# Optimization experiments

Measured on AMD Instinct MI355X. Metric: run time of the kernel, lower is better.

The kernel has to match this reference:

```python
import jax, jax.numpy as jnp
import numpy as np

B, N, D_IN, D_OUT = 16, 512, 256, 32
C_SP, H, W = 64, 256, 256


def setup_inputs() -> dict:
    key = jax.random.key(0)
    k1, k2, k3, k4, k5 = jax.random.split(key, 5)
    return {
        "spatial_info": jax.random.normal(k1, (B, C_SP, H, W), dtype=jnp.float32),
        "entity_embeddings": jax.random.normal(k2, (B, N, D_IN), dtype=jnp.float32),
        "W_proj": jax.random.normal(k3, (D_IN, D_OUT), dtype=jnp.float32) / np.sqrt(D_IN),
        "b_proj": jax.random.normal(k4, (D_OUT,), dtype=jnp.float32) * 0.01,
        "locations": jax.random.randint(k5, (B, N, 2), 0, 256, dtype=jnp.int32),
    }


def reference(spatial_info, entity_embeddings, W_proj, b_proj, locations):
    # per-entity linear projection (fc_block): [B, N, D_out]
    proj = jnp.einsum('bnd,de->bne', entity_embeddings, W_proj) + b_proj

    Bb, C, Hh, Ww = spatial_info.shape
    # clamp locations like the torch min/max logic
    h = jnp.clip(locations[..., 0], 0, Hh - 1)  # [B, N]
    w = jnp.clip(locations[..., 1], 0, Ww - 1)  # [B, N]
    flat = h * Ww + w                            # [B, N] flattened spatial index

    scatter_map = jnp.zeros((Bb, Hh * Ww, proj.shape[-1]), dtype=spatial_info.dtype)
    b_idx = jnp.arange(Bb, dtype=flat.dtype)[:, None]  # [B, 1]
    scatter_map = scatter_map.at[b_idx, flat].set(proj)
    scatter_map = scatter_map.reshape(Bb, Hh, Ww, -1).transpose(0, 3, 1, 2)  # [B, D_out, H, W]

    return jnp.concatenate([spatial_info, scatter_map], axis=1)
```

## Files before the change

### kernel.cpp

```cpp
#include <hip/hip_runtime.h>

#define BATCH 16
#define NENT  512
#define D_IN  256
#define D_OUT 32
#define CSP   64
#define COUT  96
#define HWDIM 256
#define HWSZ  65536
#define HW4   16384
#define SP_B4  (CSP * HW4)
#define SC_B4  (D_OUT * HW4)
#define OUT_B4 (COUT * HW4)

__global__ void init_proj_kernel(const float* __restrict__ emb,
                                 const float* __restrict__ Wp,
                                 const float* __restrict__ bp,
                                 int4* __restrict__ owner4,
                                 float* __restrict__ projbuf) {
    int tid = blockIdx.x * blockDim.x + threadIdx.x;
    const int NZ4 = BATCH * HWSZ / 4;
    if (tid < NZ4) {
        owner4[tid] = make_int4(0, 0, 0, 0);
        return;
    }
    int gid = tid - NZ4;
    int ent = gid >> 5;
    int e   = gid & 31;
    float acc = bp[e];
    const float* er = emb + ent * D_IN;
    #pragma unroll 8
    for (int d = 0; d < D_IN; ++d) {
        acc += er[d] * Wp[d * D_OUT + e];
    }
    projbuf[gid] = acc;
}

__global__ void owner_kernel(const int* __restrict__ loc,
                             int* __restrict__ owner) {
    int gid = blockIdx.x * blockDim.x + threadIdx.x;
    if (gid >= BATCH * NENT) return;
    int h = loc[gid * 2 + 0];
    int w = loc[gid * 2 + 1];
    h = min(max(h, 0), HWDIM - 1);
    w = min(max(w, 0), HWDIM - 1);
    int b = gid >> 9;
    int n = gid & (NENT - 1);
    atomicMax(&owner[b * HWSZ + h * HWDIM + w], n + 1);
}

__global__ void fused_out_kernel(const float4* __restrict__ sp,
                                 const int4* __restrict__ owner4,
                                 const float* __restrict__ projbuf,
                                 float4* __restrict__ out) {
    const int PER = 2048 * 256;
    int b = blockIdx.y;
    int t = blockIdx.x * blockDim.x + threadIdx.x;

    const float4* spb  = sp  + (size_t)b * SP_B4;
    float4*       outb = out + (size_t)b * OUT_B4;

    outb[t]        = spb[t];
    outb[t + PER]  = spb[t + PER];

    int e   = t >> 14;
    int hw4 = t & (HW4 - 1);
    int4 ow = owner4[b * HW4 + hw4];
    const float* pb = projbuf + b * (NENT * D_OUT) + e;
    float4 v;
    v.x = ow.x ? pb[(ow.x - 1) * D_OUT] : 0.f;
    v.y = ow.y ? pb[(ow.y - 1) * D_OUT] : 0.f;
    v.z = ow.z ? pb[(ow.z - 1) * D_OUT] : 0.f;
    v.w = ow.w ? pb[(ow.w - 1) * D_OUT] : 0.f;
    outb[SP_B4 + t] = v;
}

extern "C" void kernel_launch(void* const* d_in, const int* in_sizes, int n_in,
                              void* d_out, int out_size, void* d_ws, size_t ws_size,
                              hipStream_t stream) {
    const float* spatial = (const float*)d_in[0];
    const float* emb     = (const float*)d_in[1];
    const float* Wp      = (const float*)d_in[2];
    const float* bp      = (const float*)d_in[3];
    const int*   loc     = (const int*)d_in[4];
    float* out = (float*)d_out;

    int*   owner   = (int*)d_ws;
    float* projbuf = (float*)((char*)d_ws + BATCH * HWSZ * sizeof(int));

    init_proj_kernel<<<2048, 256, 0, stream>>>(emb, Wp, bp, (int4*)owner, projbuf);
    owner_kernel<<<32, 256, 0, stream>>>(loc, owner);
    dim3 grid(2048, BATCH);
    fused_out_kernel<<<grid, 256, 0, stream>>>((const float4*)spatial,
                                               (const int4*)owner, projbuf,
                                               (float4*)out);
}
```

Before: 143.4 us.

## Use nontemporal loads/stores for streaming copy and vectorize projection embedding loads

The spatial copy and scatter output stores now use nontemporal load/store builtins so the large streamed data bypasses cache retention. The projection GEMV reads embedding rows as float4 vectors, and the gather loads are made unconditional with a clamped index so they can be issued without branching. The aim is less cache pollution in the bandwidth-bound copy and fewer load instructions, at the cost of extra speculative gather loads for empty cells.

```diff
diff --git a/kernel.cpp b/kernel.cpp
--- a/kernel.cpp
+++ b/kernel.cpp
@@ -13,25 +13,34 @@
 #define SC_B4  (D_OUT * HW4)
 #define OUT_B4 (COUT * HW4)
 
+typedef float vfloat4 __attribute__((ext_vector_type(4)));
+typedef int   vint4   __attribute__((ext_vector_type(4)));
+
 __global__ void init_proj_kernel(const float* __restrict__ emb,
                                  const float* __restrict__ Wp,
                                  const float* __restrict__ bp,
-                                 int4* __restrict__ owner4,
+                                 vint4* __restrict__ owner4,
                                  float* __restrict__ projbuf) {
     int tid = blockIdx.x * blockDim.x + threadIdx.x;
     const int NZ4 = BATCH * HWSZ / 4;
     if (tid < NZ4) {
-        owner4[tid] = make_int4(0, 0, 0, 0);
+        vint4 z = {0, 0, 0, 0};
+        owner4[tid] = z;
         return;
     }
     int gid = tid - NZ4;
     int ent = gid >> 5;
     int e   = gid & 31;
+    const vfloat4* er4 = (const vfloat4*)(emb + (size_t)ent * D_IN);
     float acc = bp[e];
-    const float* er = emb + ent * D_IN;
     #pragma unroll 8
-    for (int d = 0; d < D_IN; ++d) {
-        acc += er[d] * Wp[d * D_OUT + e];
+    for (int d4 = 0; d4 < D_IN / 4; ++d4) {
+        vfloat4 ev = er4[d4];
+        int d = d4 * 4;
+        acc += ev.x * Wp[(d + 0) * D_OUT + e];
+        acc += ev.y * Wp[(d + 1) * D_OUT + e];
+        acc += ev.z * Wp[(d + 2) * D_OUT + e];
+        acc += ev.w * Wp[(d + 3) * D_OUT + e];
     }
     projbuf[gid] = acc;
 }
@@ -40,39 +49,43 @@
                              int* __restrict__ owner) {
     int gid = blockIdx.x * blockDim.x + threadIdx.x;
     if (gid >= BATCH * NENT) return;
-    int h = loc[gid * 2 + 0];
-    int w = loc[gid * 2 + 1];
-    h = min(max(h, 0), HWDIM - 1);
-    w = min(max(w, 0), HWDIM - 1);
+    int h = min(max(loc[gid * 2 + 0], 0), HWDIM - 1);
+    int w = min(max(loc[gid * 2 + 1], 0), HWDIM - 1);
     int b = gid >> 9;
     int n = gid & (NENT - 1);
     atomicMax(&owner[b * HWSZ + h * HWDIM + w], n + 1);
 }
 
-__global__ void fused_out_kernel(const float4* __restrict__ sp,
-                                 const int4* __restrict__ owner4,
+__global__ void fused_out_kernel(const vfloat4* __restrict__ sp,
+                                 const vint4* __restrict__ owner4,
                                  const float* __restrict__ projbuf,
-                                 float4* __restrict__ out) {
+                                 vfloat4* __restrict__ out) {
     const int PER = 2048 * 256;
     int b = blockIdx.y;
     int t = blockIdx.x * blockDim.x + threadIdx.x;
 
-    const float4* spb  = sp  + (size_t)b * SP_B4;
-    float4*       outb = out + (size_t)b * OUT_B4;
+    const vfloat4* spb  = sp  + (size_t)b * SP_B4;
+    vfloat4*       outb = out + (size_t)b * OUT_B4;
 
-    outb[t]        = spb[t];
-    outb[t + PER]  = spb[t + PER];
+    vfloat4 c0 = __builtin_nontemporal_load(&spb[t]);
+    __builtin_nontemporal_store(c0, &outb[t]);
+    vfloat4 c1 = __builtin_nontemporal_load(&spb[t + PER]);
+    __builtin_nontemporal_store(c1, &outb[t + PER]);
 
     int e   = t >> 14;
     int hw4 = t & (HW4 - 1);
-    int4 ow = owner4[b * HW4 + hw4];
+    vint4 ow = owner4[b * HW4 + hw4];
     const float* pb = projbuf + b * (NENT * D_OUT) + e;
-    float4 v;
-    v.x = ow.x ? pb[(ow.x - 1) * D_OUT] : 0.f;
-    v.y = ow.y ? pb[(ow.y - 1) * D_OUT] : 0.f;
-    v.z = ow.z ? pb[(ow.z - 1) * D_OUT] : 0.f;
-    v.w = ow.w ? pb[(ow.w - 1) * D_OUT] : 0.f;
-    outb[SP_B4 + t] = v;
+    float vx = pb[max(ow.x - 1, 0) * D_OUT];
+    float vy = pb[max(ow.y - 1, 0) * D_OUT];
+    float vz = pb[max(ow.z - 1, 0) * D_OUT];
+    float vw = pb[max(ow.w - 1, 0) * D_OUT];
+    vfloat4 v;
+    v.x = ow.x ? vx : 0.f;
+    v.y = ow.y ? vy : 0.f;
+    v.z = ow.z ? vz : 0.f;
+    v.w = ow.w ? vw : 0.f;
+    __builtin_nontemporal_store(v, &outb[SP_B4 + t]);
 }
 
 extern "C" void kernel_launch(void* const* d_in, const int* in_sizes, int n_in,
@@ -88,10 +101,10 @@
     int*   owner   = (int*)d_ws;
     float* projbuf = (float*)((char*)d_ws + BATCH * HWSZ * sizeof(int));
 
-    init_proj_kernel<<<2048, 256, 0, stream>>>(emb, Wp, bp, (int4*)owner, projbuf);
+    init_proj_kernel<<<2048, 256, 0, stream>>>(emb, Wp, bp, (vint4*)owner, projbuf);
     owner_kernel<<<32, 256, 0, stream>>>(loc, owner);
     dim3 grid(2048, BATCH);
-    fused_out_kernel<<<grid, 256, 0, stream>>>((const float4*)spatial,
-                                               (const int4*)owner, projbuf,
-                                               (float4*)out);
+    fused_out_kernel<<<grid, 256, 0, stream>>>((const vfloat4*)spatial,
+                                               (const vint4*)owner, projbuf,
+                                               (vfloat4*)out);
 }
```

New measurement: 137.1 us. -4.4%, faster.
